# Kernel tuning notes

Hardware: AMD Instinct MI355X
Metric: run time of the kernel (lower is better)

Reference implementation:

```python
import jax, jax.numpy as jnp
import numpy as np

N = 131072      # number of nodes / samples
IN_DIM = 128    # input_dim
H = 128         # hidden_dim
OUT_DIM = 10    # output_dim


def setup_inputs() -> dict:
    key = jax.random.key(0)
    ks = jax.random.split(key, 20)
    s = 0.05
    def rn(k, shape):
        return jax.random.normal(k, shape, jnp.float32) * s
    return {
        "x": jax.random.normal(ks[0], (N, IN_DIM), jnp.float32),
        # GRU layer 1 (seq_len=1, h0=0 => weight_hh contributes nothing; only b_hh matters)
        "w_ih_f1": rn(ks[1], (3 * H, IN_DIM)), "b_ih_f1": rn(ks[2], (3 * H,)), "b_hh_f1": rn(ks[3], (3 * H,)),
        "w_ih_b1": rn(ks[4], (3 * H, IN_DIM)), "b_ih_b1": rn(ks[5], (3 * H,)), "b_hh_b1": rn(ks[6], (3 * H,)),
        # GRU layer 2 (input 2H)
        "w_ih_f2": rn(ks[7], (3 * H, 2 * H)), "b_ih_f2": rn(ks[8], (3 * H,)), "b_hh_f2": rn(ks[9], (3 * H,)),
        "w_ih_b2": rn(ks[10], (3 * H, 2 * H)), "b_ih_b2": rn(ks[11], (3 * H,)), "b_hh_b2": rn(ks[12], (3 * H,)),
        # GCNConv layers
        "w_g1": rn(ks[13], (2 * H, 128)), "b_g1": rn(ks[14], (128,)),
        "w_g2": rn(ks[15], (128, 64)), "b_g2": rn(ks[16], (64,)),
        # final fc
        "w_fc": rn(ks[17], (64, OUT_DIM)), "b_fc": rn(ks[18], (OUT_DIM,)),
    }


def _gru_cell_zero(x, w_ih, b_ih, b_hh):
    # PyTorch GRU cell with h_prev = 0: h' = (1 - z) * n_gate
    gi = x @ w_ih.T + b_ih                    # [n, 3H]
    ir, iz, inn = jnp.split(gi, 3, axis=-1)
    hr, hz, hn = jnp.split(b_hh, 3)
    r = jax.nn.sigmoid(ir + hr)
    z = jax.nn.sigmoid(iz + hz)
    ng = jnp.tanh(inn + r * hn)
    return (1.0 - z) * ng


def _gcn(x, w, b, sources, targets, n):
    # PyG GCNConv: D^{-1/2}(A+I)D^{-1/2} X W + b, self-loops already in edge lists
    xw = x @ w                                 # [n, out]
    deg = jax.ops.segment_sum(jnp.ones(sources.shape[0], x.dtype), targets, num_segments=n)
    dinv = jax.lax.rsqrt(deg)
    norm = dinv[sources] * dinv[targets]       # [E]
    msg = norm[:, None] * xw[sources]          # gather
    return jax.ops.segment_sum(msg, targets, num_segments=n) + b  # scatter-add


def reference(x, w_ih_f1, b_ih_f1, b_hh_f1, w_ih_b1, b_ih_b1, b_hh_b1,
              w_ih_f2, b_ih_f2, b_hh_f2, w_ih_b2, b_ih_b2, b_hh_b2,
              w_g1, b_g1, w_g2, b_g2, w_fc, b_fc):
    n = x.shape[0]
    # seq_len = 1 => bidirectional GRU output is [fwd_cell(x); bwd_cell(x)]
    h1 = jnp.concatenate([_gru_cell_zero(x, w_ih_f1, b_ih_f1, b_hh_f1),
                          _gru_cell_zero(x, w_ih_b1, b_ih_b1, b_hh_b1)], axis=-1)
    h2 = jnp.concatenate([_gru_cell_zero(h1, w_ih_f2, b_ih_f2, b_hh_f2),
                          _gru_cell_zero(h1, w_ih_b2, b_ih_b2, b_hh_b2)], axis=-1)
    # chain graph, both directions, plus self loops (GCNConv adds them)
    src = jnp.arange(n - 1)
    dst = jnp.arange(1, n)
    ar = jnp.arange(n)
    sources = jnp.concatenate([src, dst, ar])
    targets = jnp.concatenate([dst, src, ar])
    g1 = _gcn(h2, w_g1, b_g1, sources, targets, n)   # dropout is identity in eval
    g2 = _gcn(g1, w_g2, b_g2, sources, targets, n)
    return g2 @ w_fc + b_fc
```

## Files before the change

### kernel.cpp

```cpp
#include <hip/hip_runtime.h>
#include <stdint.h>

#define N_NODES 131072
#define HDIM 128

typedef __bf16 bf16x8 __attribute__((ext_vector_type(8)));
typedef float f32x4 __attribute__((ext_vector_type(4)));
typedef unsigned short us8 __attribute__((ext_vector_type(8)));
typedef unsigned short ushort_t;

__device__ __forceinline__ float bf2f(ushort_t u) {
    union { float f; uint32_t i; } v; v.i = ((uint32_t)u) << 16; return v.f;
}
__device__ __forceinline__ ushort_t f2bf(float f) {
    union { float f; uint32_t i; } v; v.f = f;
    uint32_t i = v.i;
    return (ushort_t)((i + 0x7FFFu + ((i >> 16) & 1u)) >> 16);
}

__device__ __forceinline__ void gll16(const ushort_t* g, ushort_t* l) {
    __builtin_amdgcn_global_load_lds(
        (const __attribute__((address_space(1))) uint32_t*)g,
        (__attribute__((address_space(3))) uint32_t*)l, 16, 0, 0);
}

__device__ __forceinline__ bf16x8 ldsw(const ushort_t* base, int R, int g) {
    return *(const bf16x8*)&base[R * 64 + (((g - R) & 7) << 3)];
}

__device__ __forceinline__ float fsig(float x) {
    return __builtin_amdgcn_rcpf(1.0f + __expf(-x));
}
__device__ __forceinline__ float ftanh(float y) {
    float yc = fminf(fmaxf(y, -15.0f), 15.0f);
    float e = __expf(2.0f * yc);
    return (e - 1.0f) * __builtin_amdgcn_rcpf(e + 1.0f);
}

template<int NC>
__device__ __forceinline__ void swz(int b, int& m, int& c) {
    int mhi = b / (8 * NC);
    int rem = b - mhi * (8 * NC);
    c = rem >> 3;
    m = mhi * 8 + (rem & 7);
}

__global__ __launch_bounds__(256) void prep_weights(
    const float* __restrict__ w_f1, const float* __restrict__ w_b1,
    const float* __restrict__ w_f2, const float* __restrict__ w_b2,
    ushort_t* __restrict__ PWF1, ushort_t* __restrict__ PWB1,
    ushort_t* __restrict__ PWF2, ushort_t* __restrict__ PWB2,
    float* __restrict__ Zc)
{
    int idx = blockIdx.x * 256 + threadIdx.x;
    if (idx < 49152) {
        PWF1[idx] = f2bf(w_f1[idx]);
    } else if (idx < 98304) {
        int j = idx - 49152;  PWB1[j] = f2bf(w_b1[j]);
    } else if (idx < 196608) {
        int j = idx - 98304;  PWF2[j] = f2bf(w_f2[j]);
    } else if (idx < 294912) {
        int j = idx - 196608; PWB2[j] = f2bf(w_b2[j]);
    }
    float4 z4; z4.x = 0.0f; z4.y = 0.0f; z4.z = 0.0f; z4.w = 0.0f;
    for (int i = idx; i < 327680; i += 294912) ((float4*)Zc)[i] = z4;
}

__global__ __launch_bounds__(256) void prep_M(
    const float* __restrict__ w_g1, const float* __restrict__ b_g1,
    const float* __restrict__ w_g2, const float* __restrict__ b_g2,
    const float* __restrict__ w_fc, const float* __restrict__ b_fc,
    ushort_t* __restrict__ M16, float* __restrict__ cc)
{
    __shared__ float wfc_s[640];
    __shared__ float T1[128][10];
    const int t = threadIdx.x;
    for (int i = t; i < 640; i += 256) wfc_s[i] = w_fc[i];
    __syncthreads();
    if (t < 128) {
        float s[10];
        #pragma unroll
        for (int j = 0; j < 10; ++j) s[j] = 0.0f;
        const float4* row = (const float4*)(w_g2 + t * 64);
        #pragma unroll
        for (int k4 = 0; k4 < 16; ++k4) {
            float4 v = row[k4];
            #pragma unroll
            for (int j = 0; j < 10; ++j)
                s[j] += v.x * wfc_s[(k4 * 4 + 0) * 10 + j] + v.y * wfc_s[(k4 * 4 + 1) * 10 + j]
                      + v.z * wfc_s[(k4 * 4 + 2) * 10 + j] + v.w * wfc_s[(k4 * 4 + 3) * 10 + j];
        }
        #pragma unroll
        for (int j = 0; j < 10; ++j) T1[t][j] = s[j];
    }
    __syncthreads();
    float m[10];
    #pragma unroll
    for (int j = 0; j < 10; ++j) m[j] = 0.0f;
    const float4* row1 = (const float4*)(w_g1 + t * 128);
    #pragma unroll 4
    for (int k4 = 0; k4 < 32; ++k4) {
        float4 v = row1[k4];
        #pragma unroll
        for (int j = 0; j < 10; ++j)
            m[j] += v.x * T1[k4 * 4 + 0][j] + v.y * T1[k4 * 4 + 1][j]
                  + v.z * T1[k4 * 4 + 2][j] + v.w * T1[k4 * 4 + 3][j];
    }
    #pragma unroll
    for (int j = 0; j < 16; ++j)
        M16[j * 256 + t] = (j < 10) ? f2bf(m[j]) : (ushort_t)0;
    if (t < 10) {
        float s1 = 0.0f;
        for (int k2 = 0; k2 < 128; ++k2) s1 += b_g1[k2] * T1[k2][t];
        cc[t] = s1;
        float s2 = 0.0f;
        for (int k3 = 0; k3 < 64; ++k3) s2 += b_g2[k3] * wfc_s[k3 * 10 + t];
        cc[16 + t] = s2 + b_fc[t];
    }
}

__global__ __launch_bounds__(256, 4) void gru_l1(
    const float* __restrict__ X,
    const ushort_t* __restrict__ Wf,
    const ushort_t* __restrict__ Wb,
    const float* __restrict__ bi_f, const float* __restrict__ bh_f,
    const float* __restrict__ bi_b, const float* __restrict__ bh_b,
    ushort_t* __restrict__ Hout)
{
    __shared__ ushort_t As[128 * 64];
    __shared__ ushort_t Bs[96 * 64];
    const int tid = threadIdx.x;
    int mt, comb;
    swz<8>(blockIdx.x, mt, comb);
    const int m0 = mt * 128;
    const int dir = comb >> 2;
    const int j0 = (comb & 3) * 32;
    const ushort_t* W = dir ? Wb : Wf;
    const float* b_ih = dir ? bi_b : bi_f;
    const float* b_hh = dir ? bh_b : bh_f;
    const int coloff = dir << 7;

    const int wv = tid >> 6, lane = tid & 63;
    const int lr = lane & 15, lq = lane >> 4;
    const int tr = tid >> 3, tc = tid & 7;
    const int sc = ((tr + tc) & 7) << 3;

    f32x4 acc[3][2][2];
    #pragma unroll
    for (int g = 0; g < 3; ++g)
        #pragma unroll
        for (int rt = 0; rt < 2; ++rt)
            #pragma unroll
            for (int ct = 0; ct < 2; ++ct)
                #pragma unroll
                for (int e = 0; e < 4; ++e) acc[g][rt][ct][e] = 0.0f;

    for (int t = 0; t < 2; ++t) {
        const int k0 = t * 64;
        const float* ga = X + (size_t)(m0 + tr) * 128 + k0 + sc;
        float4 fa[4][2];
        #pragma unroll
        for (int i = 0; i < 4; ++i) {
            const float4* p = (const float4*)(ga + (size_t)i * 32 * 128);
            fa[i][0] = p[0]; fa[i][1] = p[1];
        }
        #pragma unroll
        for (int i = 0; i < 3; ++i) {
            int wr = (i << 7) + j0 + tr;
            gll16(W + (size_t)wr * 128 + k0 + sc, &Bs[(i * 256 + tid) * 8]);
        }
        #pragma unroll
        for (int i = 0; i < 4; ++i) {
            us8 t8;
            t8[0] = f2bf(fa[i][0].x); t8[1] = f2bf(fa[i][0].y);
            t8[2] = f2bf(fa[i][0].z); t8[3] = f2bf(fa[i][0].w);
            t8[4] = f2bf(fa[i][1].x); t8[5] = f2bf(fa[i][1].y);
            t8[6] = f2bf(fa[i][1].z); t8[7] = f2bf(fa[i][1].w);
            *(us8*)&As[(i * 256 + tid) * 8] = t8;
        }
        __syncthreads();
        #pragma unroll
        for (int kk = 0; kk < 64; kk += 32) {
            const int g8 = (kk >> 3) + lq;
            bf16x8 a0 = ldsw(As, wv * 32 + lr, g8);
            bf16x8 a1 = ldsw(As, wv * 32 + 16 + lr, g8);
            #pragma unroll
            for (int g = 0; g < 3; ++g) {
                #pragma unroll
                for (int ct = 0; ct < 2; ++ct) {
                    bf16x8 b = ldsw(Bs, g * 32 + ct * 16 + lr, g8);
                    acc[g][0][ct] = __builtin_amdgcn_mfma_f32_16x16x32_bf16(a0, b, acc[g][0][ct], 0, 0, 0);
                    acc[g][1][ct] = __builtin_amdgcn_mfma_f32_16x16x32_bf16(a1, b, acc[g][1][ct], 0, 0, 0);
                }
            }
        }
        __syncthreads();
    }

    #pragma unroll
    for (int ct = 0; ct < 2; ++ct) {
        const int j = j0 + ct * 16 + lr;
        const float br  = b_ih[j] + b_hh[j];
        const float bz  = b_ih[HDIM + j] + b_hh[HDIM + j];
        const float bn  = b_ih[2 * HDIM + j];
        const float bhn = b_hh[2 * HDIM + j];
        #pragma unroll
        for (int rt = 0; rt < 2; ++rt) {
            #pragma unroll
            for (int r = 0; r < 4; ++r) {
                const int row = m0 + wv * 32 + rt * 16 + lq * 4 + r;
                float rg = fsig(acc[0][rt][ct][r] + br);
                float zg = fsig(acc[1][rt][ct][r] + bz);
                float ng = ftanh(acc[2][rt][ct][r] + bn + rg * bhn);
                Hout[(size_t)row * 256 + coloff + j] = f2bf((1.0f - zg) * ng);
            }
        }
    }
}

__global__ __launch_bounds__(256, 5) void gru_l2(
    const ushort_t* __restrict__ A,
    const ushort_t* __restrict__ Wf,
    const ushort_t* __restrict__ Wb,
    const float* __restrict__ bi_f, const float* __restrict__ bh_f,
    const float* __restrict__ bi_b, const float* __restrict__ bh_b,
    const ushort_t* __restrict__ M16,
    float* __restrict__ Zc)
{
    __shared__ ushort_t As[128 * 64];
    __shared__ ushort_t Bs[96 * 64];
    const int tid = threadIdx.x;
    int mt, comb;
    swz<8>(blockIdx.x, mt, comb);
    const int m0 = mt * 128;
    const int dir = comb >> 2;
    const int j0 = (comb & 3) * 32;
    const ushort_t* W = dir ? Wb : Wf;
    const float* b_ih = dir ? bi_b : bi_f;
    const float* b_hh = dir ? bh_b : bh_f;
    const int coloff = dir << 7;

    const int wv = tid >> 6, lane = tid & 63;
    const int lr = lane & 15, lq = lane >> 4;
    const int tr = tid >> 3, tc = tid & 7;
    const int sc = ((tr + tc) & 7) << 3;

    f32x4 acc[3][2][2];
    #pragma unroll
    for (int g = 0; g < 3; ++g)
        #pragma unroll
        for (int rt = 0; rt < 2; ++rt)
            #pragma unroll
            for (int ct = 0; ct < 2; ++ct)
                #pragma unroll
                for (int e = 0; e < 4; ++e) acc[g][rt][ct][e] = 0.0f;

    for (int t = 0; t < 4; ++t) {
        const int k0 = t * 64;
        const ushort_t* ga = A + (size_t)(m0 + tr) * 256 + k0 + sc;
        #pragma unroll
        for (int i = 0; i < 4; ++i)
            gll16(ga + (size_t)i * 32 * 256, &As[(i * 256 + tid) * 8]);
        #pragma unroll
        for (int i = 0; i < 3; ++i) {
            int wr = (i << 7) + j0 + tr;
            gll16(W + (size_t)wr * 256 + k0 + sc, &Bs[(i * 256 + tid) * 8]);
        }
        __syncthreads();
        #pragma unroll
        for (int kk = 0; kk < 64; kk += 32) {
            const int g8 = (kk >> 3) + lq;
            bf16x8 a0 = ldsw(As, wv * 32 + lr, g8);
            bf16x8 a1 = ldsw(As, wv * 32 + 16 + lr, g8);
            #pragma unroll
            for (int g = 0; g < 3; ++g) {
                #pragma unroll
                for (int ct = 0; ct < 2; ++ct) {
                    bf16x8 b = ldsw(Bs, g * 32 + ct * 16 + lr, g8);
                    acc[g][0][ct] = __builtin_amdgcn_mfma_f32_16x16x32_bf16(a0, b, acc[g][0][ct], 0, 0, 0);
                    acc[g][1][ct] = __builtin_amdgcn_mfma_f32_16x16x32_bf16(a1, b, acc[g][1][ct], 0, 0, 0);
                }
            }
        }
        __syncthreads();
    }

    const bf16x8 mb = *(const bf16x8*)&M16[lr * 256 + coloff + j0 + lq * 8];

    #pragma unroll
    for (int ct = 0; ct < 2; ++ct) {
        const int j = j0 + ct * 16 + lr;
        const float br  = b_ih[j] + b_hh[j];
        const float bz  = b_ih[HDIM + j] + b_hh[HDIM + j];
        const float bn  = b_ih[2 * HDIM + j];
        const float bhn = b_hh[2 * HDIM + j];
        #pragma unroll
        for (int rt = 0; rt < 2; ++rt) {
            #pragma unroll
            for (int r = 0; r < 4; ++r) {
                const int lrow = wv * 32 + rt * 16 + lq * 4 + r;
                float rg = fsig(acc[0][rt][ct][r] + br);
                float zg = fsig(acc[1][rt][ct][r] + bz);
                float ng = ftanh(acc[2][rt][ct][r] + bn + rg * bhn);
                As[lrow * 32 + ct * 16 + lr] = f2bf((1.0f - zg) * ng);
            }
        }
    }

    bf16x8 ha0 = *(const bf16x8*)&As[(wv * 32 + lr) * 32 + lq * 8];
    bf16x8 ha1 = *(const bf16x8*)&As[(wv * 32 + 16 + lr) * 32 + lq * 8];
    f32x4 z0, z1;
    #pragma unroll
    for (int e = 0; e < 4; ++e) { z0[e] = 0.0f; z1[e] = 0.0f; }
    z0 = __builtin_amdgcn_mfma_f32_16x16x32_bf16(ha0, mb, z0, 0, 0, 0);
    z1 = __builtin_amdgcn_mfma_f32_16x16x32_bf16(ha1, mb, z1, 0, 0, 0);

    if (lr < 10) {
        #pragma unroll
        for (int r = 0; r < 4; ++r) {
            atomicAdd(&Zc[(size_t)(m0 + wv * 32 + lq * 4 + r) * 10 + lr], z0[r]);
            atomicAdd(&Zc[(size_t)(m0 + wv * 32 + 16 + lq * 4 + r) * 10 + lr], z1[r]);
        }
    }
}

__device__ __forceinline__ float dcoef(int i) {
    return (i == 0 || i == N_NODES - 1) ? 0.70710678118654752f : 0.57735026918962576f;
}
__global__ __launch_bounds__(256) void st5(
    const float* __restrict__ z, float* __restrict__ out,
    const float* __restrict__ cc)
{
    int idx = blockIdx.x * 256 + threadIdx.x;
    int i = idx >> 4, c = idx & 15;
    if (c >= 10) return;
    float d_i = dcoef(i);
    float accv = 0.0f, dsum = d_i;
    #pragma unroll
    for (int oj = -1; oj <= 1; ++oj) {
        int j = i + oj;
        if (j < 0 || j >= N_NODES) continue;
        float dj = dcoef(j);
        if (oj != 0) dsum += dj;
        float wj = 0.0f;
        #pragma unroll
        for (int ok = -1; ok <= 1; ++ok) {
            int k = j + ok;
            if (k < 0 || k >= N_NODES) continue;
            wj += dcoef(k) * z[(size_t)k * 10 + c];
        }
        accv += dj * dj * wj;
    }
    out[(size_t)i * 10 + c] = d_i * accv + d_i * dsum * cc[c] + cc[16 + c];
}

extern "C" void kernel_launch(void* const* d_in, const int* in_sizes, int n_in,
                              void* d_out, int out_size, void* d_ws, size_t ws_size,
                              hipStream_t stream) {
    const float* x     = (const float*)d_in[0];
    const float* w_f1  = (const float*)d_in[1];
    const float* bi_f1 = (const float*)d_in[2];
    const float* bh_f1 = (const float*)d_in[3];
    const float* w_b1  = (const float*)d_in[4];
    const float* bi_b1 = (const float*)d_in[5];
    const float* bh_b1 = (const float*)d_in[6];
    const float* w_f2  = (const float*)d_in[7];
    const float* bi_f2 = (const float*)d_in[8];
    const float* bh_f2 = (const float*)d_in[9];
    const float* w_b2  = (const float*)d_in[10];
    const float* bi_b2 = (const float*)d_in[11];
    const float* bh_b2 = (const float*)d_in[12];
    const float* w_g1  = (const float*)d_in[13];
    const float* b_g1  = (const float*)d_in[14];
    const float* w_g2  = (const float*)d_in[15];
    const float* b_g2  = (const float*)d_in[16];
    const float* w_fc  = (const float*)d_in[17];
    const float* b_fc  = (const float*)d_in[18];

    char* ws = (char*)d_ws;
    ushort_t* h1   = (ushort_t*)(ws);
    float*    Zc   = (float*)(ws + 67108864);
    ushort_t* PWF1 = (ushort_t*)(ws + 134217728);
    ushort_t* PWB1 = PWF1 + 49152;
    ushort_t* PWF2 = PWB1 + 49152;
    ushort_t* PWB2 = PWF2 + 98304;
    ushort_t* M16  = PWB2 + 98304;
    float*    cc   = (float*)(M16 + 4096);

    prep_weights<<<1152, 256, 0, stream>>>(w_f1, w_b1, w_f2, w_b2,
                                           PWF1, PWB1, PWF2, PWB2, Zc);
    prep_M<<<1, 256, 0, stream>>>(w_g1, b_g1, w_g2, b_g2, w_fc, b_fc, M16, cc);

    gru_l1<<<N_NODES / 128 * 8, 256, 0, stream>>>(
        x, PWF1, PWB1, bi_f1, bh_f1, bi_b1, bh_b1, h1);
    gru_l2<<<N_NODES / 128 * 8, 256, 0, stream>>>(
        h1, PWF2, PWB2, bi_f2, bh_f2, bi_b2, bh_b2, M16, Zc);

    st5<<<N_NODES * 16 / 256, 256, 0, stream>>>(Zc, (float*)d_out, cc);
}
```

Measured before the change: 298.1 us.

## Replace atomic accumulation of projected outputs with per-slice partials plus reduction

gru_l2 no longer atomically adds its 10-wide projected contributions into a shared zeroed buffer. Each of the 8 column/direction combos now writes plain stores into its own slice, and a new zsum kernel adds the 8 slices. This removes atomic contention and the zero-init pass. The cost is an extra launch and roughly 40 MB of extra partial-buffer traffic. The hidden-state staging in LDS also moves to a padded per-wave region with a block barrier before the readback.

```diff
diff --git a/kernel.cpp b/kernel.cpp
--- a/kernel.cpp
+++ b/kernel.cpp
@@ -49,8 +49,7 @@
     const float* __restrict__ w_f1, const float* __restrict__ w_b1,
     const float* __restrict__ w_f2, const float* __restrict__ w_b2,
     ushort_t* __restrict__ PWF1, ushort_t* __restrict__ PWB1,
-    ushort_t* __restrict__ PWF2, ushort_t* __restrict__ PWB2,
-    float* __restrict__ Zc)
+    ushort_t* __restrict__ PWF2, ushort_t* __restrict__ PWB2)
 {
     int idx = blockIdx.x * 256 + threadIdx.x;
     if (idx < 49152) {
@@ -62,8 +61,6 @@
     } else if (idx < 294912) {
         int j = idx - 196608; PWB2[j] = f2bf(w_b2[j]);
     }
-    float4 z4; z4.x = 0.0f; z4.y = 0.0f; z4.z = 0.0f; z4.w = 0.0f;
-    for (int i = idx; i < 327680; i += 294912) ((float4*)Zc)[i] = z4;
 }
 
 __global__ __launch_bounds__(256) void prep_M(
@@ -225,7 +222,7 @@
     const float* __restrict__ bi_f, const float* __restrict__ bh_f,
     const float* __restrict__ bi_b, const float* __restrict__ bh_b,
     const ushort_t* __restrict__ M16,
-    float* __restrict__ Zc)
+    float* __restrict__ Zp)
 {
     __shared__ ushort_t As[128 * 64];
     __shared__ ushort_t Bs[96 * 64];
@@ -287,6 +284,7 @@
 
     const bf16x8 mb = *(const bf16x8*)&M16[lr * 256 + coloff + j0 + lq * 8];
 
+    ushort_t* hs = &As[wv * 1280];
     #pragma unroll
     for (int ct = 0; ct < 2; ++ct) {
         const int j = j0 + ct * 16 + lr;
@@ -298,17 +296,18 @@
         for (int rt = 0; rt < 2; ++rt) {
             #pragma unroll
             for (int r = 0; r < 4; ++r) {
-                const int lrow = wv * 32 + rt * 16 + lq * 4 + r;
+                const int lrow = rt * 16 + lq * 4 + r;
                 float rg = fsig(acc[0][rt][ct][r] + br);
                 float zg = fsig(acc[1][rt][ct][r] + bz);
                 float ng = ftanh(acc[2][rt][ct][r] + bn + rg * bhn);
-                As[lrow * 32 + ct * 16 + lr] = f2bf((1.0f - zg) * ng);
+                hs[lrow * 40 + ct * 16 + lr] = f2bf((1.0f - zg) * ng);
             }
         }
     }
-
-    bf16x8 ha0 = *(const bf16x8*)&As[(wv * 32 + lr) * 32 + lq * 8];
-    bf16x8 ha1 = *(const bf16x8*)&As[(wv * 32 + 16 + lr) * 32 + lq * 8];
+    __syncthreads();
+
+    bf16x8 ha0 = *(const bf16x8*)&hs[lr * 40 + lq * 8];
+    bf16x8 ha1 = *(const bf16x8*)&hs[(16 + lr) * 40 + lq * 8];
     f32x4 z0, z1;
     #pragma unroll
     for (int e = 0; e < 4; ++e) { z0[e] = 0.0f; z1[e] = 0.0f; }
@@ -316,12 +315,26 @@
     z1 = __builtin_amdgcn_mfma_f32_16x16x32_bf16(ha1, mb, z1, 0, 0, 0);
 
     if (lr < 10) {
+        float* zslice = Zp + (size_t)comb * (N_NODES * 10);
         #pragma unroll
         for (int r = 0; r < 4; ++r) {
-            atomicAdd(&Zc[(size_t)(m0 + wv * 32 + lq * 4 + r) * 10 + lr], z0[r]);
-            atomicAdd(&Zc[(size_t)(m0 + wv * 32 + 16 + lq * 4 + r) * 10 + lr], z1[r]);
-        }
-    }
+            zslice[(size_t)(m0 + wv * 32 + lq * 4 + r) * 10 + lr] = z0[r];
+            zslice[(size_t)(m0 + wv * 32 + 16 + lq * 4 + r) * 10 + lr] = z1[r];
+        }
+    }
+}
+
+__global__ __launch_bounds__(256) void zsum(
+    const float4* __restrict__ Zp4, float4* __restrict__ Zc4)
+{
+    int i = blockIdx.x * 256 + threadIdx.x;
+    float4 a = Zp4[i];
+    #pragma unroll
+    for (int s = 1; s < 8; ++s) {
+        float4 b = Zp4[(size_t)s * 327680 + i];
+        a.x += b.x; a.y += b.y; a.z += b.z; a.w += b.w;
+    }
+    Zc4[i] = a;
 }
 
 __device__ __forceinline__ float dcoef(int i) {
@@ -379,7 +392,8 @@
 
     char* ws = (char*)d_ws;
     ushort_t* h1   = (ushort_t*)(ws);
-    float*    Zc   = (float*)(ws + 67108864);
+    float*    Zp   = (float*)(ws + 67108864);
+    float*    Zc   = (float*)(ws + 109051904);
     ushort_t* PWF1 = (ushort_t*)(ws + 134217728);
     ushort_t* PWB1 = PWF1 + 49152;
     ushort_t* PWF2 = PWB1 + 49152;
@@ -388,13 +402,14 @@
     float*    cc   = (float*)(M16 + 4096);
 
     prep_weights<<<1152, 256, 0, stream>>>(w_f1, w_b1, w_f2, w_b2,
-                                           PWF1, PWB1, PWF2, PWB2, Zc);
+                                           PWF1, PWB1, PWF2, PWB2);
     prep_M<<<1, 256, 0, stream>>>(w_g1, b_g1, w_g2, b_g2, w_fc, b_fc, M16, cc);
 
     gru_l1<<<N_NODES / 128 * 8, 256, 0, stream>>>(
         x, PWF1, PWB1, bi_f1, bh_f1, bi_b1, bh_b1, h1);
     gru_l2<<<N_NODES / 128 * 8, 256, 0, stream>>>(
-        h1, PWF2, PWB2, bi_f2, bh_f2, bi_b2, bh_b2, M16, Zc);
-
+        h1, PWF2, PWB2, bi_f2, bh_f2, bi_b2, bh_b2, M16, Zp);
+
+    zsum<<<1280, 256, 0, stream>>>((const float4*)Zp, (float4*)Zc);
     st5<<<N_NODES * 16 / 256, 256, 0, stream>>>(Zc, (float*)d_out, cc);
 }
```

After: 278.1 us. 1.07x faster.
